# Kernel optimization log

Measured on AMD Instinct MI355X. Metric: run time of the kernel, lower is better.

Reference implementation:

```python
import jax, jax.numpy as jnp
import numpy as np

B, N_SPINS, D_MODEL, K_MC = 256, 128, 768, 25


def setup_inputs() -> dict:
    key = jax.random.key(0)
    k1, k2, k3 = jax.random.split(key, 3)
    features = jax.random.normal(k1, (B, N_SPINS, D_MODEL), dtype=jnp.float32)
    coalitions = jax.random.randint(k2, (K_MC, N_SPINS), 0, 2, dtype=jnp.int32)
    w_v = jax.random.normal(k3, (D_MODEL, D_MODEL), dtype=jnp.float32) * 0.02
    scale = jnp.full((1,), 0.1, dtype=jnp.float32)
    return {"features": features, "coalitions": coalitions, "w_v": w_v, "scale": scale}


def reference(features, coalitions, w_v, scale):
    # features: [B, n, d]; coalitions: [K, n] in {0,1}; w_v: [d, d]; scale: [1]
    c = coalitions.astype(features.dtype)                      # [K, n]
    # coalition_value batched over all K coalitions at once:
    # sum_j mask[k,j] * features[b,j,:]  (sum and linear proj commute)
    s = jnp.einsum('kn,bnd->bkd', c, features)                 # [B, K, d]
    proj = s @ w_v                                             # [B, K, d]
    norm = jnp.linalg.norm(proj, axis=-1)                      # [B, K]
    cv = jax.nn.relu(norm * scale[0])                          # coalition values [B, K]
    # Shapley estimate: mean(v | i in S) - mean(v | i not in S)
    cnt_with = c.sum(axis=0)                                   # [n]
    cnt_without = c.shape[0] - cnt_with
    v_with = (cv @ c) / jnp.maximum(cnt_with, 1.0)             # [B, n]
    v_without = (cv @ (1.0 - c)) / jnp.maximum(cnt_without, 1.0)
    valid = (cnt_with > 0) & (cnt_without > 0)                 # [n]
    shapley = jnp.where(valid, v_with - v_without, 0.0)        # [B, n]
    return shapley
```

## Files before the change

kernel.cpp:

```cpp
#include <hip/hip_runtime.h>
#include <hip/hip_bf16.h>
#include <stdint.h>

#define NB  256
#define NSP 128
#define DM  768
#define KMC 25
#define MROWS (NB*KMC)

#define OFF_S    0u
#define OFF_WT   9830400u
#define OFF_N2   11010048u
#define OFF_COEF 11035648u
#define OFF_CB   11049984u

typedef __attribute__((ext_vector_type(8))) short bf16x8;
typedef __attribute__((ext_vector_type(4))) float f32x4;
typedef unsigned int u32;

#define GLOAD_LDS16(gp, lp) \
  __builtin_amdgcn_global_load_lds((const __attribute__((address_space(1))) u32*)(gp), \
                                   (__attribute__((address_space(3))) u32*)(lp), 16, 0, 0)

#define KA_WAITV_BAR(N) asm volatile("s_waitcnt vmcnt(" #N ")\n\ts_barrier" ::: "memory")
#define KA_BAR()        asm volatile("s_waitcnt lgkmcnt(0)\n\ts_barrier" ::: "memory")

__global__ __launch_bounds__(256) void prep_kernel(const float* __restrict__ wv,
                                                   const int* __restrict__ co,
                                                   char* __restrict__ ws) {
  const int blk = blockIdx.x;
  const int t = threadIdx.x;
  if (blk < 144) {
    __shared__ __hip_bfloat16 lt[64][66];
    const int bi = blk / 12, bj = blk % 12;
    const int k0 = bi * 64, n0 = bj * 64;
    #pragma unroll
    for (int i = 0; i < 16; ++i) {
      int idx = t + i * 256;
      int r = idx >> 6, c = idx & 63;
      lt[c][r] = __float2bfloat16(wv[(size_t)(k0 + r) * DM + n0 + c]);
    }
    __syncthreads();
    __hip_bfloat16* wT = (__hip_bfloat16*)(ws + OFF_WT);
    #pragma unroll
    for (int i = 0; i < 16; ++i) {
      int idx = t + i * 256;
      int r = idx >> 6, c = idx & 63;
      wT[(size_t)(n0 + r) * DM + k0 + c] = lt[r][c];
    }
  } else if (blk == 144) {
    if (t < NSP) {
      const int n = t;
      int cw = 0;
      #pragma unroll
      for (int k = 0; k < KMC; ++k) cw += co[k * NSP + n];
      const int cwo = KMC - cw;
      const bool valid = (cw > 0) && (cwo > 0);
      float* coefT = (float*)(ws + OFF_COEF);
      #pragma unroll
      for (int k = 0; k < 28; ++k) {
        float v = 0.f;
        if (valid && k < KMC) v = co[k * NSP + n] ? (1.f / (float)cw) : (-1.f / (float)cwo);
        coefT[n * 28 + k] = v;
      }
    }
  } else if (blk < 170) {
    int i = (blk - 145) * 256 + t;
    if (i < MROWS) ((float*)(ws + OFF_N2))[i] = 0.f;
  } else {
    int k = blk - 170;
    if (t < NSP) {
      float v = (k < KMC) ? (float)co[k * NSP + t] : 0.f;
      ((__hip_bfloat16*)(ws + OFF_CB))[k * NSP + t] = __float2bfloat16(v);
    }
  }
}

__global__ __launch_bounds__(256, 3) void kA(const float* __restrict__ f,
                                             const __hip_bfloat16* __restrict__ Cb,
                                             __hip_bfloat16* __restrict__ s) {
  const int b = blockIdx.x;
  const int slice = blockIdx.y;
  const int tid = threadIdx.x;
  const int w = tid >> 6;
  const int lane = tid & 63;
  const int lo = lane & 15, hi = lane >> 4;

  __shared__ __align__(16) float Fs[4][16 * 192];

  bf16x8 A0[4], A1[4];
  #pragma unroll
  for (int ks = 0; ks < 4; ++ks) {
    A0[ks] = *(const bf16x8*)(Cb + (size_t)lo * NSP + ks * 32 + hi * 8);
    A1[ks] = *(const bf16x8*)(Cb + (size_t)(16 + lo) * NSP + ks * 32 + hi * 8);
  }
  asm volatile("s_waitcnt vmcnt(0)" ::: "memory");

  int goff[3];
  #pragma unroll
  for (int q = 0; q < 3; ++q) {
    int e = (w * 3 + q) * 256 + lane * 4;
    int r = e / 192, c = e - r * 192;
    goff[q] = r * DM + c;
  }

  const float* fb = f + (size_t)b * NSP * DM + slice * 192;

  f32x4 ac0[3], ac1[3];
  #pragma unroll
  for (int ct = 0; ct < 3; ++ct)
    #pragma unroll
    for (int i = 0; i < 4; ++i) { ac0[ct][i] = 0.f; ac1[ct][i] = 0.f; }

#define KA_ISSUE(ck, bi) { \
    const float* fp_ = fb + (size_t)(ck) * 16 * DM; \
    _Pragma("unroll") for (int q = 0; q < 3; ++q) \
      GLOAD_LDS16(fp_ + goff[q], (char*)&Fs[(bi)][0] + ((w * 3 + q) << 10)); }

#define KA_MFMAPAIR(ks, blo, bhi) { \
    const float* Fb_ = (hi >> 1) ? &Fs[(bhi)][0] : &Fs[(blo)][0]; \
    const int rb_ = (hi & 1) * 8; \
    _Pragma("unroll") for (int ct = 0; ct < 3; ++ct) { \
      bf16x8 Bf; \
      _Pragma("unroll") for (int j = 0; j < 8; ++j) { \
        float v_ = Fb_[(rb_ + j) * 192 + w * 48 + ct * 16 + lo]; \
        __hip_bfloat16 h_ = __float2bfloat16(v_); \
        Bf[j] = *(short*)&h_; } \
      ac0[ct] = __builtin_amdgcn_mfma_f32_16x16x32_bf16(A0[ks], Bf, ac0[ct], 0, 0, 0); \
      ac1[ct] = __builtin_amdgcn_mfma_f32_16x16x32_bf16(A1[ks], Bf, ac1[ct], 0, 0, 0); } }

  KA_ISSUE(0, 0) KA_ISSUE(1, 1) KA_ISSUE(2, 2) KA_ISSUE(3, 3)
  KA_WAITV_BAR(6);
  KA_MFMAPAIR(0, 0, 1)
  KA_BAR();
  KA_ISSUE(4, 0) KA_ISSUE(5, 1)
  KA_WAITV_BAR(6);
  KA_MFMAPAIR(1, 2, 3)
  KA_BAR();
  KA_ISSUE(6, 2) KA_ISSUE(7, 3)
  KA_WAITV_BAR(6);
  KA_MFMAPAIR(2, 0, 1)
  KA_WAITV_BAR(0);
  KA_MFMAPAIR(3, 2, 3)

#undef KA_ISSUE
#undef KA_MFMAPAIR

  #pragma unroll
  for (int ct = 0; ct < 3; ++ct) {
    int dcol = slice * 192 + w * 48 + ct * 16 + lo;
    #pragma unroll
    for (int i = 0; i < 4; ++i) {
      int r0 = hi * 4 + i;
      s[((size_t)b * KMC + r0) * DM + dcol] = __float2bfloat16(ac0[ct][i]);
      int r1 = 16 + hi * 4 + i;
      if (r1 < KMC)
        s[((size_t)b * KMC + r1) * DM + dcol] = __float2bfloat16(ac1[ct][i]);
    }
  }
}

#define BM 128
#define BN 192
#define BK 32
#define NTK 24

__global__ __launch_bounds__(256) void kB(char* __restrict__ ws) {
  const int bid = blockIdx.x;
  const int tm = bid >> 2;
  const int tn = bid & 3;
  const int tid = threadIdx.x;
  const int wid = tid >> 6;
  const int lane = tid & 63;
  const int wm = wid >> 1;
  const int wn = wid & 1;

  const __hip_bfloat16* S  = (const __hip_bfloat16*)(ws + OFF_S);
  const __hip_bfloat16* WT = (const __hip_bfloat16*)(ws + OFF_WT);
  float* norm2 = (float*)(ws + OFF_N2);

  __shared__ __align__(16) char As[2][BM * BK * 2];
  __shared__ __align__(16) char Bs[2][BN * BK * 2];

  const char* gA[2]; char *lA0[2], *lA1[2];
  #pragma unroll
  for (int j = 0; j < 2; ++j) {
    int li = (wid * 2 + j) * 64 + lane;
    int r = li >> 2, sl = li & 3;
    int slx = sl ^ ((r >> 1) & 3);
    gA[j] = (const char*)(S + (size_t)(tm * BM + r) * DM) + slx * 16;
    lA0[j] = As[0] + (wid * 2 + j) * 1024;
    lA1[j] = As[1] + (wid * 2 + j) * 1024;
  }
  const char* gB[3]; char *lB0[3], *lB1[3];
  #pragma unroll
  for (int j = 0; j < 3; ++j) {
    int li = (wid * 3 + j) * 64 + lane;
    int r = li >> 2, sl = li & 3;
    int slx = sl ^ ((r >> 1) & 3);
    gB[j] = (const char*)(WT + (size_t)(tn * BN + r) * DM) + slx * 16;
    lB0[j] = Bs[0] + (wid * 3 + j) * 1024;
    lB1[j] = Bs[1] + (wid * 3 + j) * 1024;
  }

  auto stage = [&](int tk, int bsel) {
    size_t koff = (size_t)tk * (BK * 2);
    #pragma unroll
    for (int j = 0; j < 2; ++j) GLOAD_LDS16(gA[j] + koff, bsel ? lA1[j] : lA0[j]);
    #pragma unroll
    for (int j = 0; j < 3; ++j) GLOAD_LDS16(gB[j] + koff, bsel ? lB1[j] : lB0[j]);
  };

  f32x4 acc[4][6];
  #pragma unroll
  for (int m = 0; m < 4; ++m)
    #pragma unroll
    for (int n = 0; n < 6; ++n)
      #pragma unroll
      for (int j = 0; j < 4; ++j) acc[m][n][j] = 0.f;

  int offA[4], offB[6];
  #pragma unroll
  for (int m = 0; m < 4; ++m) {
    int r = wm * 64 + m * 16 + (lane & 15);
    int sl = (lane >> 4) ^ ((r >> 1) & 3);
    offA[m] = r * 64 + sl * 16;
  }
  #pragma unroll
  for (int n = 0; n < 6; ++n) {
    int r = wn * 96 + n * 16 + (lane & 15);
    int sl = (lane >> 4) ^ ((r >> 1) & 3);
    offB[n] = r * 64 + sl * 16;
  }

  stage(0, 0);
  for (int tk = 0; tk < NTK; ++tk) {
    int cur = tk & 1;
    __syncthreads();
    if (tk + 1 < NTK) stage(tk + 1, cur ^ 1);
    bf16x8 af[4], bfr[6];
    #pragma unroll
    for (int m = 0; m < 4; ++m) af[m] = *(const bf16x8*)(As[cur] + offA[m]);
    #pragma unroll
    for (int n = 0; n < 6; ++n) bfr[n] = *(const bf16x8*)(Bs[cur] + offB[n]);
    #pragma unroll
    for (int m = 0; m < 4; ++m)
      #pragma unroll
      for (int n = 0; n < 6; ++n)
        acc[m][n] = __builtin_amdgcn_mfma_f32_16x16x32_bf16(af[m], bfr[n], acc[m][n], 0, 0, 0);
  }

  float ps[4][4];
  #pragma unroll
  for (int m = 0; m < 4; ++m)
    #pragma unroll
    for (int i = 0; i < 4; ++i) {
      float v = 0.f;
      #pragma unroll
      for (int n = 0; n < 6; ++n) { float x = acc[m][n][i]; v += x * x; }
      #pragma unroll
      for (int d = 1; d < 16; d <<= 1) v += __shfl_xor(v, d, 64);
      ps[m][i] = v;
    }
  if ((lane & 15) == 0) {
    int g = lane >> 4;
    #pragma unroll
    for (int m = 0; m < 4; ++m)
      #pragma unroll
      for (int i = 0; i < 4; ++i)
        atomicAdd(&norm2[tm * BM + wm * 64 + m * 16 + g * 4 + i], ps[m][i]);
  }
}

__global__ __launch_bounds__(128) void kC(const char* __restrict__ ws,
                                          const float* __restrict__ scale,
                                          float* __restrict__ out) {
  const int b = blockIdx.x, n = threadIdx.x;
  const float* norm2 = (const float*)(ws + OFF_N2);
  const float* coefT = (const float*)(ws + OFF_COEF);
  __shared__ float cvs[32];
  if (n < KMC) {
    float nv = norm2[b * KMC + n];
    cvs[n] = fmaxf(sqrtf(fmaxf(nv, 0.f)) * scale[0], 0.f);
  } else if (n < 32) {
    cvs[n] = 0.f;
  }
  __syncthreads();
  float sum = 0.f;
  #pragma unroll
  for (int k = 0; k < KMC; ++k) sum += cvs[k] * coefT[n * 28 + k];
  out[b * NSP + n] = sum;
}

extern "C" void kernel_launch(void* const* d_in, const int* in_sizes, int n_in,
                              void* d_out, int out_size, void* d_ws, size_t ws_size,
                              hipStream_t stream) {
  const float* features   = (const float*)d_in[0];
  const int*   coalitions = (const int*)d_in[1];
  const float* wv         = (const float*)d_in[2];
  const float* scale      = (const float*)d_in[3];
  char* ws = (char*)d_ws;

  prep_kernel<<<202, 256, 0, stream>>>(wv, coalitions, ws);
  dim3 gaa(NB, 4);
  kA<<<gaa, 256, 0, stream>>>(features, (const __hip_bfloat16*)(ws + OFF_CB),
                              (__hip_bfloat16*)(ws + OFF_S));
  kB<<<200, 256, 0, stream>>>(ws);
  kC<<<NB, 128, 0, stream>>>(ws, scale, (float*)d_out);
}
```

Measured before the change: 51.79 us.

## Restructure kA to full-row 512-thread blocks and halve kB M-tile

kA now runs one 512-thread block per batch covering all 768 columns instead of four 192-column slices. It uses a 3-stage LDS ring with padded row stride (770) in a new issue/compute schedule, reducing per-block overhead and possibly LDS bank conflicts. kB's M tile shrinks from 128 to 64 rows, doubling the grid to 400 blocks to better fill the CUs, at the cost of re-reading the W tiles more often and issuing more atomics.

```diff
diff --git a/kernel.cpp b/kernel.cpp
--- a/kernel.cpp
+++ b/kernel.cpp
@@ -76,17 +76,18 @@
   }
 }
 
-__global__ __launch_bounds__(256, 3) void kA(const float* __restrict__ f,
+#define KAP 770
+
+__global__ __launch_bounds__(512, 2) void kA(const float* __restrict__ f,
                                              const __hip_bfloat16* __restrict__ Cb,
                                              __hip_bfloat16* __restrict__ s) {
   const int b = blockIdx.x;
-  const int slice = blockIdx.y;
   const int tid = threadIdx.x;
   const int w = tid >> 6;
   const int lane = tid & 63;
   const int lo = lane & 15, hi = lane >> 4;
 
-  __shared__ __align__(16) float Fs[4][16 * 192];
+  __shared__ __align__(16) float Fs[3][16 * KAP];
 
   bf16x8 A0[4], A1[4];
   #pragma unroll
@@ -96,59 +97,62 @@
   }
   asm volatile("s_waitcnt vmcnt(0)" ::: "memory");
 
-  int goff[3];
-  #pragma unroll
-  for (int q = 0; q < 3; ++q) {
-    int e = (w * 3 + q) * 256 + lane * 4;
-    int r = e / 192, c = e - r * 192;
-    goff[q] = r * DM + c;
-  }
-
-  const float* fb = f + (size_t)b * NSP * DM + slice * 192;
-
-  f32x4 ac0[3], ac1[3];
-  #pragma unroll
-  for (int ct = 0; ct < 3; ++ct)
+  int gofs[6], lofs[6];
+  #pragma unroll
+  for (int q = 0; q < 6; ++q) {
+    int rq = q / 3, sg = q - rq * 3;
+    int rr = 2 * w + rq;
+    gofs[q] = rr * DM + sg * 256 + lane * 4;
+    lofs[q] = rr * (KAP * 4) + sg * 1024;
+  }
+
+  const float* fb = f + (size_t)b * NSP * DM;
+
+  f32x4 ac0[6], ac1[6];
+  #pragma unroll
+  for (int ct = 0; ct < 6; ++ct)
     #pragma unroll
     for (int i = 0; i < 4; ++i) { ac0[ct][i] = 0.f; ac1[ct][i] = 0.f; }
 
 #define KA_ISSUE(ck, bi) { \
     const float* fp_ = fb + (size_t)(ck) * 16 * DM; \
-    _Pragma("unroll") for (int q = 0; q < 3; ++q) \
-      GLOAD_LDS16(fp_ + goff[q], (char*)&Fs[(bi)][0] + ((w * 3 + q) << 10)); }
-
-#define KA_MFMAPAIR(ks, blo, bhi) { \
+    _Pragma("unroll") for (int q = 0; q < 6; ++q) \
+      GLOAD_LDS16(fp_ + gofs[q], (char*)&Fs[(bi)][0] + lofs[q]); }
+
+#define KA_MFMA(ks, blo, bhi) { \
     const float* Fb_ = (hi >> 1) ? &Fs[(bhi)][0] : &Fs[(blo)][0]; \
     const int rb_ = (hi & 1) * 8; \
-    _Pragma("unroll") for (int ct = 0; ct < 3; ++ct) { \
+    _Pragma("unroll") for (int ct = 0; ct < 6; ++ct) { \
       bf16x8 Bf; \
       _Pragma("unroll") for (int j = 0; j < 8; ++j) { \
-        float v_ = Fb_[(rb_ + j) * 192 + w * 48 + ct * 16 + lo]; \
+        float v_ = Fb_[(rb_ + j) * KAP + w * 96 + ct * 16 + lo]; \
         __hip_bfloat16 h_ = __float2bfloat16(v_); \
         Bf[j] = *(short*)&h_; } \
       ac0[ct] = __builtin_amdgcn_mfma_f32_16x16x32_bf16(A0[ks], Bf, ac0[ct], 0, 0, 0); \
       ac1[ct] = __builtin_amdgcn_mfma_f32_16x16x32_bf16(A1[ks], Bf, ac1[ct], 0, 0, 0); } }
 
-  KA_ISSUE(0, 0) KA_ISSUE(1, 1) KA_ISSUE(2, 2) KA_ISSUE(3, 3)
+  KA_ISSUE(0, 0) KA_ISSUE(1, 1) KA_ISSUE(2, 2)
   KA_WAITV_BAR(6);
-  KA_MFMAPAIR(0, 0, 1)
+  KA_MFMA(0, 0, 1)
   KA_BAR();
-  KA_ISSUE(4, 0) KA_ISSUE(5, 1)
+  KA_ISSUE(3, 0) KA_ISSUE(4, 1)
   KA_WAITV_BAR(6);
-  KA_MFMAPAIR(1, 2, 3)
+  KA_MFMA(1, 2, 0)
   KA_BAR();
-  KA_ISSUE(6, 2) KA_ISSUE(7, 3)
+  KA_ISSUE(5, 2) KA_ISSUE(6, 0)
   KA_WAITV_BAR(6);
-  KA_MFMAPAIR(2, 0, 1)
+  KA_MFMA(2, 1, 2)
+  KA_BAR();
+  KA_ISSUE(7, 1)
   KA_WAITV_BAR(0);
-  KA_MFMAPAIR(3, 2, 3)
+  KA_MFMA(3, 0, 1)
 
 #undef KA_ISSUE
-#undef KA_MFMAPAIR
-
-  #pragma unroll
-  for (int ct = 0; ct < 3; ++ct) {
-    int dcol = slice * 192 + w * 48 + ct * 16 + lo;
+#undef KA_MFMA
+
+  #pragma unroll
+  for (int ct = 0; ct < 6; ++ct) {
+    int dcol = w * 96 + ct * 16 + lo;
     #pragma unroll
     for (int i = 0; i < 4; ++i) {
       int r0 = hi * 4 + i;
@@ -160,7 +164,7 @@
   }
 }
 
-#define BM 128
+#define BM 64
 #define BN 192
 #define BK 32
 #define NTK 24
@@ -182,15 +186,14 @@
   __shared__ __align__(16) char As[2][BM * BK * 2];
   __shared__ __align__(16) char Bs[2][BN * BK * 2];
 
-  const char* gA[2]; char *lA0[2], *lA1[2];
-  #pragma unroll
-  for (int j = 0; j < 2; ++j) {
-    int li = (wid * 2 + j) * 64 + lane;
+  const char* gA; char *lAA0, *lAA1;
+  {
+    int li = wid * 64 + lane;
     int r = li >> 2, sl = li & 3;
     int slx = sl ^ ((r >> 1) & 3);
-    gA[j] = (const char*)(S + (size_t)(tm * BM + r) * DM) + slx * 16;
-    lA0[j] = As[0] + (wid * 2 + j) * 1024;
-    lA1[j] = As[1] + (wid * 2 + j) * 1024;
+    gA = (const char*)(S + (size_t)(tm * BM + r) * DM) + slx * 16;
+    lAA0 = As[0] + wid * 1024;
+    lAA1 = As[1] + wid * 1024;
   }
   const char* gB[3]; char *lB0[3], *lB1[3];
   #pragma unroll
@@ -205,24 +208,23 @@
 
   auto stage = [&](int tk, int bsel) {
     size_t koff = (size_t)tk * (BK * 2);
-    #pragma unroll
-    for (int j = 0; j < 2; ++j) GLOAD_LDS16(gA[j] + koff, bsel ? lA1[j] : lA0[j]);
+    GLOAD_LDS16(gA + koff, bsel ? lAA1 : lAA0);
     #pragma unroll
     for (int j = 0; j < 3; ++j) GLOAD_LDS16(gB[j] + koff, bsel ? lB1[j] : lB0[j]);
   };
 
-  f32x4 acc[4][6];
-  #pragma unroll
-  for (int m = 0; m < 4; ++m)
+  f32x4 acc[2][6];
+  #pragma unroll
+  for (int m = 0; m < 2; ++m)
     #pragma unroll
     for (int n = 0; n < 6; ++n)
       #pragma unroll
       for (int j = 0; j < 4; ++j) acc[m][n][j] = 0.f;
 
-  int offA[4], offB[6];
-  #pragma unroll
-  for (int m = 0; m < 4; ++m) {
-    int r = wm * 64 + m * 16 + (lane & 15);
+  int offA[2], offB[6];
+  #pragma unroll
+  for (int m = 0; m < 2; ++m) {
+    int r = wm * 32 + m * 16 + (lane & 15);
     int sl = (lane >> 4) ^ ((r >> 1) & 3);
     offA[m] = r * 64 + sl * 16;
   }
@@ -238,21 +240,21 @@
     int cur = tk & 1;
     __syncthreads();
     if (tk + 1 < NTK) stage(tk + 1, cur ^ 1);
-    bf16x8 af[4], bfr[6];
-    #pragma unroll
-    for (int m = 0; m < 4; ++m) af[m] = *(const bf16x8*)(As[cur] + offA[m]);
+    bf16x8 af[2], bfr[6];
+    #pragma unroll
+    for (int m = 0; m < 2; ++m) af[m] = *(const bf16x8*)(As[cur] + offA[m]);
     #pragma unroll
     for (int n = 0; n < 6; ++n) bfr[n] = *(const bf16x8*)(Bs[cur] + offB[n]);
     #pragma unroll
-    for (int m = 0; m < 4; ++m)
+    for (int m = 0; m < 2; ++m)
       #pragma unroll
       for (int n = 0; n < 6; ++n)
         acc[m][n] = __builtin_amdgcn_mfma_f32_16x16x32_bf16(af[m], bfr[n], acc[m][n], 0, 0, 0);
   }
 
-  float ps[4][4];
-  #pragma unroll
-  for (int m = 0; m < 4; ++m)
+  float ps[2][4];
+  #pragma unroll
+  for (int m = 0; m < 2; ++m)
     #pragma unroll
     for (int i = 0; i < 4; ++i) {
       float v = 0.f;
@@ -265,10 +267,10 @@
   if ((lane & 15) == 0) {
     int g = lane >> 4;
     #pragma unroll
-    for (int m = 0; m < 4; ++m)
+    for (int m = 0; m < 2; ++m)
       #pragma unroll
       for (int i = 0; i < 4; ++i)
-        atomicAdd(&norm2[tm * BM + wm * 64 + m * 16 + g * 4 + i], ps[m][i]);
+        atomicAdd(&norm2[tm * BM + wm * 32 + m * 16 + g * 4 + i], ps[m][i]);
   }
 }
 
@@ -302,9 +304,8 @@
   char* ws = (char*)d_ws;
 
   prep_kernel<<<202, 256, 0, stream>>>(wv, coalitions, ws);
-  dim3 gaa(NB, 4);
-  kA<<<gaa, 256, 0, stream>>>(features, (const __hip_bfloat16*)(ws + OFF_CB),
-                              (__hip_bfloat16*)(ws + OFF_S));
-  kB<<<200, 256, 0, stream>>>(ws);
+  kA<<<NB, 512, 0, stream>>>(features, (const __hip_bfloat16*)(ws + OFF_CB),
+                             (__hip_bfloat16*)(ws + OFF_S));
+  kB<<<400, 256, 0, stream>>>(ws);
   kC<<<NB, 128, 0, stream>>>(ws, scale, (float*)d_out);
 }
```

After: 46.42 us. -10.4%, faster.
